# Kernel optimization log

Measured on AMD Instinct MI355X. Metric: run time of the kernel, lower is better.

## Reference

```python
import jax, jax.numpy as jnp
import numpy as np

D_MODEL = 96
D_INNER = 192   # ssm_ratio * d_model
R = 6           # dt_rank = ceil(96/16)
DH = 32         # d_inner // dt_rank (per-head dim)
K = 4           # scan directions
N = 16          # d_state
EPS = 1e-5


def setup_inputs() -> dict:
    key = jax.random.key(0)
    ks = jax.random.split(key, 10)
    B, H, W = 8, 64, 64
    f = lambda k, s, sc: jax.random.normal(k, s, jnp.float32) * sc
    return dict(
        x=jax.random.normal(ks[0], (B, H, W, D_MODEL), jnp.float32),
        w_in=f(ks[1], (D_MODEL, D_INNER), 0.02),
        w_conv=f(ks[2], (3, 3, 1, D_INNER), 0.1),      # depthwise HWIO
        b_conv=f(ks[3], (D_INNER,), 0.1),
        x_proj_weight=f(ks[4], (K, R + 2 * N, D_INNER), 0.02),
        A_logs=f(ks[5], (K, R), 0.5),
        Ds=jnp.ones((K, R, DH), jnp.float32),
        dt_bias=0.1 * jax.random.uniform(ks[6], (K, R), jnp.float32),
        ln_g=jnp.ones((D_INNER,), jnp.float32),
        ln_b=jnp.zeros((D_INNER,), jnp.float32),
        w_out=f(ks[7], (D_INNER, D_MODEL), 0.02),
    )


def _cross_scan(x):
    # x: (B,H,W,C) -> (B,L,4,C): [row-major, col-major, rev row, rev col]
    B, H, W, C = x.shape
    x0 = x.reshape(B, H * W, C)
    x1 = jnp.transpose(x, (0, 2, 1, 3)).reshape(B, H * W, C)
    return jnp.stack([x0, x1, x0[:, ::-1], x1[:, ::-1]], axis=2)


def _cross_merge(ys, H, W):
    # ys: (B,L,4,C) -> (B,L,C) summed after undoing each scan order
    B, L, _, C = ys.shape
    y_row = ys[:, :, 0] + ys[:, :, 2][:, ::-1]
    y_col = ys[:, :, 1] + ys[:, :, 3][:, ::-1]
    y_col = jnp.transpose(y_col.reshape(B, W, H, C), (0, 2, 1, 3)).reshape(B, L, C)
    return y_row + y_col


def _selective_scan(us, dts, As, Bs, Cs, Dsr, dtb):
    # us:(B,L,KR,DH) dts:(B,L,KR) As:(KR,) Bs,Cs:(B,L,K,N) Dsr:(KR,DH) dtb:(KR,)
    dt = jax.nn.softplus(dts + dtb)                 # (B,L,KR)
    decay = jnp.exp(dt * As)                        # (B,L,KR)
    xu = dt[..., None] * us                         # (B,L,KR,DH)
    Bh = jnp.repeat(Bs, R, axis=2)                  # (B,L,KR,N) head h -> group h//R
    Ch = jnp.repeat(Cs, R, axis=2)
    B_, L, KR, _ = us.shape
    tfirst = lambda a: jnp.moveaxis(a, 1, 0)

    def step(h, inp):
        dec, xu_t, b_t, c_t = inp                   # (B,KR),(B,KR,DH),(B,KR,N),(B,KR,N)
        h = dec[:, :, None, None] * h + xu_t[..., None] * b_t[:, :, None, :]
        y = jnp.einsum('bkdn,bkn->bkd', h, c_t)
        return h, y

    h0 = jnp.zeros((B_, KR, DH, N), us.dtype)
    _, ys = jax.lax.scan(step, h0, (tfirst(decay), tfirst(xu), tfirst(Bh), tfirst(Ch)))
    ys = jnp.moveaxis(ys, 0, 1)                     # (B,L,KR,DH)
    return ys + us * Dsr                            # skip term D*u


def reference(x, w_in, w_conv, b_conv, x_proj_weight, A_logs, Ds, dt_bias, ln_g, ln_b, w_out):
    B, H, W, _ = x.shape
    L = H * W
    xi = x @ w_in                                   # in_proj (no bias)
    xi = jax.lax.conv_general_dilated(
        xi, w_conv, (1, 1), 'SAME', feature_group_count=D_INNER,
        dimension_numbers=('NHWC', 'HWIO', 'NHWC')) + b_conv
    xi = jax.nn.silu(xi)
    xs = _cross_scan(xi)                            # (B,L,4,D_INNER)
    x_dbl = jnp.einsum('blkd,kcd->blkc', xs, x_proj_weight)
    dts = x_dbl[..., :R].reshape(B, L, K * R)
    Bs = x_dbl[..., R:R + N]                        # (B,L,K,N)
    Cs = x_dbl[..., R + N:]
    us = xs.reshape(B, L, K * R, DH)
    As = -jnp.exp(A_logs.astype(jnp.float32)).reshape(K * R)
    Dsr = Ds.reshape(K * R, DH)
    dtb = dt_bias.reshape(K * R)
    ys = _selective_scan(us, dts, As, Bs, Cs, Dsr, dtb)   # (B,L,KR,DH)
    y = _cross_merge(ys.reshape(B, L, K, R * DH), H, W)   # (B,L,D_INNER)
    mu = y.mean(-1, keepdims=True)
    var = ((y - mu) ** 2).mean(-1, keepdims=True)
    y = (y - mu) / jnp.sqrt(var + EPS) * ln_g + ln_b
    y = y.reshape(B, H, W, D_INNER)
    return y @ w_out                                # out_proj (no bias)
```

## Files before the change

### kernel.cpp

```cpp
#include <hip/hip_runtime.h>
#include <hip/hip_bf16.h>

#define BB 8
#define LL 4096
#define DM 96
#define DI 192
#define RRR 6
#define DHH 32
#define KKK 4
#define NNN 16
#define KRR 24
#define NCH 64
#define TT 64
#define RST 48

__device__ __forceinline__ float softplus_f(float x){
    float ax = fabsf(x);
    return fmaxf(x, 0.f) + __logf(1.f + __expf(-ax));
}
__device__ __forceinline__ float silu_f(float x){ return x / (1.f + __expf(-x)); }

__global__ void k0p(const float* __restrict__ W, const float* __restrict__ g,
                    const float* __restrict__ bta, const float* __restrict__ w_out,
                    float* __restrict__ WpR, float* __restrict__ wg, float* __restrict__ sgbw){
    int i = blockIdx.x * 256 + threadIdx.x;
    if (i < DI * 160){
        int d = i / 160, cc = i % 160; int gq = cc / 40, nc = cc % 40;
        int dir = (gq == 0) ? 0 : (gq == 1) ? 2 : (gq == 2) ? 1 : 3;
        float v = 0.f;
        if (nc < 6) v = W[(dir * 38 + nc) * DI + d];
        else if (nc >= 8) v = W[(dir * 38 + (nc - 2)) * DI + d];
        WpR[i] = v;
    } else if (i < DI * 160 + DI * DM){
        int j = i - DI * 160; int c = j / DM;
        wg[j] = w_out[j] * g[c];
    } else if (i < DI * 160 + DI * DM + DM){
        int m = i - (DI * 160 + DI * DM);
        float s = 0.f, t = 0.f;
        for (int c = 0; c < DI; ++c){
            float w = w_out[c * DM + m];
            s = fmaf(g[c], w, s);
            t = fmaf(bta[c], w, t);
        }
        sgbw[m] = s; sgbw[DM + m] = t;
    }
}

__global__ __launch_bounds__(384) void k1_inproj(const float* __restrict__ x,
                                                 const float* __restrict__ w_in,
                                                 float* __restrict__ xw){
    __shared__ float xT[DM][68];
    int pix0 = blockIdx.x * 64;
    for (int i = threadIdx.x; i < 64 * DM; i += 384){
        int c = i % DM, p = i / DM;
        xT[c][p] = x[(size_t)(pix0 + p) * DM + c];
    }
    __syncthreads();
    int cg = threadIdx.x % 48, pg = threadIdx.x / 48;
    int p0 = pg * 8;
    float4 acc[8];
    #pragma unroll
    for (int i = 0; i < 8; ++i) acc[i] = make_float4(0.f, 0.f, 0.f, 0.f);
    const float* wcol = w_in + cg * 4;
    for (int d = 0; d < DM; ++d){
        float4 w4 = *(const float4*)(wcol + d * DI);
        float4 xa = *(const float4*)(&xT[d][p0]);
        float4 xb = *(const float4*)(&xT[d][p0 + 4]);
        float xs[8] = {xa.x, xa.y, xa.z, xa.w, xb.x, xb.y, xb.z, xb.w};
        #pragma unroll
        for (int pi = 0; pi < 8; ++pi){
            acc[pi].x = fmaf(xs[pi], w4.x, acc[pi].x);
            acc[pi].y = fmaf(xs[pi], w4.y, acc[pi].y);
            acc[pi].z = fmaf(xs[pi], w4.z, acc[pi].z);
            acc[pi].w = fmaf(xs[pi], w4.w, acc[pi].w);
        }
    }
    #pragma unroll
    for (int pi = 0; pi < 8; ++pi)
        *(float4*)(xw + (size_t)(pix0 + p0 + pi) * DI + cg * 4) = acc[pi];
}

__global__ void k2_conv(const float* __restrict__ xw, const float* __restrict__ wc,
                        const float* __restrict__ bc, float* __restrict__ xi,
                        float* __restrict__ xiT){
    int gid = blockIdx.x * 256 + threadIdx.x;
    int c4 = gid % 48; int pix = gid / 48;
    int b = pix >> 12; int l = pix & 4095; int h = l >> 6; int w = l & 63;
    int c = c4 * 4;
    float4 acc = *(const float4*)(bc + c);
    #pragma unroll
    for (int dh = 0; dh < 3; ++dh){
        int hh = h + dh - 1; if ((unsigned)hh >= 64u) continue;
        #pragma unroll
        for (int dw = 0; dw < 3; ++dw){
            int ww2 = w + dw - 1; if ((unsigned)ww2 >= 64u) continue;
            float4 tap = *(const float4*)(xw + (size_t)((b << 12) + (hh << 6) + ww2) * DI + c);
            float4 wv  = *(const float4*)(wc + (dh * 3 + dw) * DI + c);
            acc.x = fmaf(tap.x, wv.x, acc.x);
            acc.y = fmaf(tap.y, wv.y, acc.y);
            acc.z = fmaf(tap.z, wv.z, acc.z);
            acc.w = fmaf(tap.w, wv.w, acc.w);
        }
    }
    acc.x = silu_f(acc.x); acc.y = silu_f(acc.y); acc.z = silu_f(acc.z); acc.w = silu_f(acc.w);
    *(float4*)(xi + (size_t)pix * DI + c) = acc;
    int lT = ((l & 63) << 6) | (l >> 6);
    *(float4*)(xiT + (size_t)((b << 12) + lT) * DI + c) = acc;
}

__global__ __launch_bounds__(320) void k3seq(const float* __restrict__ xi,
                                             const float* __restrict__ xiT,
                                             const float* __restrict__ WpR,
                                             const float* __restrict__ A_logs,
                                             const float* __restrict__ dtb,
                                             float* __restrict__ rec){
    __shared__ float xT[DI][65];
    int pass = blockIdx.y, b = blockIdx.z;
    const float* src = (pass ? xiT : xi) + (((size_t)b) << 12) * DI;
    int p0blk = blockIdx.x * 64;
    for (int i = threadIdx.x; i < 64 * DI; i += 320){
        int c = i % DI, p = i / DI;
        xT[c][p] = src[(size_t)(p0blk + p) * DI + c];
    }
    __syncthreads();
    int kg = threadIdx.x % 20, pg = threadIdx.x / 20;
    int p0 = pg * 4;
    float4 acc[4];
    #pragma unroll
    for (int i = 0; i < 4; ++i) acc[i] = make_float4(0.f, 0.f, 0.f, 0.f);
    const float* wcol = WpR + pass * 80 + kg * 4;
    for (int d = 0; d < DI; ++d){
        float4 w4 = *(const float4*)(wcol + d * 160);
        float4 xv = *(const float4*)(&xT[d][p0]);
        float xs[4] = {xv.x, xv.y, xv.z, xv.w};
        #pragma unroll
        for (int pi = 0; pi < 4; ++pi){
            acc[pi].x = fmaf(xs[pi], w4.x, acc[pi].x);
            acc[pi].y = fmaf(xs[pi], w4.y, acc[pi].y);
            acc[pi].z = fmaf(xs[pi], w4.z, acc[pi].z);
            acc[pi].w = fmaf(xs[pi], w4.w, acc[pi].w);
        }
    }
    int gq = kg / 10;
    int dir = (pass == 0) ? (gq == 0 ? 0 : 2) : (gq == 0 ? 1 : 3);
    int nc0 = (kg % 10) * 4;
    float* rb = rec + (size_t)(b * KKK + dir) * LL * RST;
    float A0, A1, A2, A3, b0, b1, b2, b3;
    if (nc0 == 0){
        A0 = -__expf(A_logs[dir * RRR + 0]); b0 = dtb[dir * RRR + 0];
        A1 = -__expf(A_logs[dir * RRR + 1]); b1 = dtb[dir * RRR + 1];
        A2 = -__expf(A_logs[dir * RRR + 2]); b2 = dtb[dir * RRR + 2];
        A3 = -__expf(A_logs[dir * RRR + 3]); b3 = dtb[dir * RRR + 3];
    } else if (nc0 == 4){
        A0 = -__expf(A_logs[dir * RRR + 4]); b0 = dtb[dir * RRR + 4];
        A1 = -__expf(A_logs[dir * RRR + 5]); b1 = dtb[dir * RRR + 5];
    }
    #pragma unroll
    for (int pi = 0; pi < 4; ++pi){
        int gp = p0blk + p0 + pi;
        int t = (dir < 2) ? gp : (LL - 1 - gp);
        float* rw = rb + (size_t)t * RST;
        float4 v = acc[pi];
        if (nc0 == 0){
            float4 dt4, dc4;
            dt4.x = softplus_f(v.x + b0); dc4.x = __expf(dt4.x * A0);
            dt4.y = softplus_f(v.y + b1); dc4.y = __expf(dt4.y * A1);
            dt4.z = softplus_f(v.z + b2); dc4.z = __expf(dt4.z * A2);
            dt4.w = softplus_f(v.w + b3); dc4.w = __expf(dt4.w * A3);
            *(float4*)(rw + 0) = dt4;
            *(float4*)(rw + 8) = dc4;
        } else if (nc0 == 4){
            float4 dt4, dc4;
            dt4.x = softplus_f(v.x + b0); dc4.x = __expf(dt4.x * A0);
            dt4.y = softplus_f(v.y + b1); dc4.y = __expf(dt4.y * A1);
            dt4.z = 0.f; dt4.w = 0.f; dc4.z = 0.f; dc4.w = 0.f;
            *(float4*)(rw + 4)  = dt4;
            *(float4*)(rw + 12) = dc4;
        } else {
            *(float4*)(rw + nc0 + 8) = v;
        }
    }
}

__global__ __launch_bounds__(192) void k4a(const float* __restrict__ xi, const float* __restrict__ xiT,
                                           const float* __restrict__ rec,
                                           float* __restrict__ Pb, float* __restrict__ Sb){
    int chunk = blockIdx.x, k = blockIdx.y, b = blockIdx.z;
    int r = threadIdx.x >> 5, d = threadIdx.x & 31;
    int kr = k * RRR + r;
    const float* rp = rec + ((size_t)(b * KKK + k) * LL + chunk * TT) * RST;
    const float* xb = ((k & 1) ? xiT : xi) + (((size_t)b) << 12) * DI + r * DHH + d;
    const float* up; ptrdiff_t ust;
    if (k < 2){ up = xb + (size_t)(chunk * TT) * DI;          ust = DI;  }
    else      { up = xb + (size_t)(LL - 1 - chunk * TT) * DI; ust = -(ptrdiff_t)DI; }
    float h[NNN];
    #pragma unroll
    for (int n = 0; n < NNN; ++n) h[n] = 0.f;
    float P = 1.f;
    #pragma unroll 4
    for (int tt = 0; tt < TT; ++tt){
        float dt  = rp[r];
        float dec = rp[8 + r];
        float u = *up;
        float xu = dt * u;
        P *= dec;
        float Bv[NNN];
        *(float4*)(Bv + 0)  = *(const float4*)(rp + 16);
        *(float4*)(Bv + 4)  = *(const float4*)(rp + 20);
        *(float4*)(Bv + 8)  = *(const float4*)(rp + 24);
        *(float4*)(Bv + 12) = *(const float4*)(rp + 28);
        #pragma unroll
        for (int n = 0; n < NNN; ++n) h[n] = fmaf(dec, h[n], xu * Bv[n]);
        rp += RST; up += ust;
    }
    size_t sb = (((size_t)(b * KRR + kr) * NCH + chunk) * DHH + d) * NNN;
    #pragma unroll
    for (int n = 0; n < NNN; ++n) Sb[sb + n] = h[n];
    if (d == 0) Pb[(size_t)(b * KRR + kr) * NCH + chunk] = P;
}

__global__ __launch_bounds__(512) void k4b(const float* __restrict__ Pb, float* __restrict__ Sb){
    int scan = blockIdx.x;
    int tid = threadIdx.x;
    size_t base = (size_t)scan * NCH * 512 + tid;
    const float* Pp = Pb + (size_t)scan * NCH;
    float s[NCH];
    #pragma unroll
    for (int c = 0; c < NCH; ++c) s[c] = Sb[base + (size_t)c * 512];
    float hb = 0.f;
    #pragma unroll
    for (int c = 0; c < NCH; ++c){
        float nv = fmaf(Pp[c], hb, s[c]);
        Sb[base + (size_t)c * 512] = hb;
        hb = nv;
    }
}

__global__ __launch_bounds__(192) void k4c(const float* __restrict__ xi, const float* __restrict__ xiT,
                                           const float* __restrict__ rec,
                                           const float* __restrict__ Ds, const float* __restrict__ Sb,
                                           __hip_bfloat16* __restrict__ ybuf){
    int chunk = blockIdx.x, k = blockIdx.y, b = blockIdx.z;
    int r = threadIdx.x >> 5, d = threadIdx.x & 31;
    int kr = k * RRR + r;
    float Dv = Ds[kr * DHH + d];
    float h[NNN];
    size_t sb = (((size_t)(b * KRR + kr) * NCH + chunk) * DHH + d) * NNN;
    #pragma unroll
    for (int n = 0; n < NNN; ++n) h[n] = Sb[sb + n];
    const float* rp = rec + ((size_t)(b * KKK + k) * LL + chunk * TT) * RST;
    const float* xb = ((k & 1) ? xiT : xi) + (((size_t)b) << 12) * DI + r * DHH + d;
    const float* up; ptrdiff_t ust;
    if (k < 2){ up = xb + (size_t)(chunk * TT) * DI;          ust = DI;  }
    else      { up = xb + (size_t)(LL - 1 - chunk * TT) * DI; ust = -(ptrdiff_t)DI; }
    __hip_bfloat16* yp = ybuf + ((size_t)(k * BB + b) * LL + chunk * TT) * DI + r * DHH + d;
    #pragma unroll 2
    for (int tt = 0; tt < TT; ++tt){
        float dt  = rp[r];
        float dec = rp[8 + r];
        float u = *up;
        float xu = dt * u;
        float Bv[NNN], Cv[NNN];
        *(float4*)(Bv + 0)  = *(const float4*)(rp + 16);
        *(float4*)(Bv + 4)  = *(const float4*)(rp + 20);
        *(float4*)(Bv + 8)  = *(const float4*)(rp + 24);
        *(float4*)(Bv + 12) = *(const float4*)(rp + 28);
        *(float4*)(Cv + 0)  = *(const float4*)(rp + 32);
        *(float4*)(Cv + 4)  = *(const float4*)(rp + 36);
        *(float4*)(Cv + 8)  = *(const float4*)(rp + 40);
        *(float4*)(Cv + 12) = *(const float4*)(rp + 44);
        float y = 0.f;
        #pragma unroll
        for (int n = 0; n < NNN; ++n){
            h[n] = fmaf(dec, h[n], xu * Bv[n]);
            y = fmaf(h[n], Cv[n], y);
        }
        y = fmaf(u, Dv, y);
        *yp = __float2bfloat16(y);
        rp += RST; up += ust; yp += DI;
    }
}

__global__ __launch_bounds__(256) void k5_out(const __hip_bfloat16* __restrict__ ybuf,
                       const float* __restrict__ wg, const float* __restrict__ sgbw,
                       float* __restrict__ out){
    __shared__ float yT[DI][36];
    __shared__ float rsL[32], rmL[32];
    int pix0 = blockIdx.x * 32;
    int b = pix0 >> 12;
    int l0 = pix0 & 4095;
    const __hip_bfloat16* y0 = ybuf + (size_t)(0 * BB + b) * LL * DI;
    const __hip_bfloat16* y1 = ybuf + (size_t)(1 * BB + b) * LL * DI;
    const __hip_bfloat16* y2 = ybuf + (size_t)(2 * BB + b) * LL * DI;
    const __hip_bfloat16* y3 = ybuf + (size_t)(3 * BB + b) * LL * DI;
    for (int i = threadIdx.x; i < 32 * DI; i += 256){
        int c = i % DI, p = i / DI;
        int l = l0 + p; int hh = l >> 6, ww = l & 63;
        int lT = (ww << 6) | hh;
        float s = __bfloat162float(y0[(size_t)l * DI + c])
                + __bfloat162float(y2[(size_t)(LL - 1 - l) * DI + c])
                + __bfloat162float(y1[(size_t)lT * DI + c])
                + __bfloat162float(y3[(size_t)(LL - 1 - lT) * DI + c]);
        yT[c][p] = s;
    }
    __syncthreads();
    {
        int p = threadIdx.x >> 3, cg = threadIdx.x & 7;
        float s = 0.f, s2 = 0.f;
        for (int c = cg; c < DI; c += 8){ float v = yT[c][p]; s += v; s2 = fmaf(v, v, s2); }
        s += __shfl_xor(s, 1, 64); s2 += __shfl_xor(s2, 1, 64);
        s += __shfl_xor(s, 2, 64); s2 += __shfl_xor(s2, 2, 64);
        s += __shfl_xor(s, 4, 64); s2 += __shfl_xor(s2, 4, 64);
        if (cg == 0){
            float mu = s * (1.f / DI);
            float var = s2 * (1.f / DI) - mu * mu;
            float rs = rsqrtf(var + 1e-5f);
            rsL[p] = rs; rmL[p] = rs * mu;
        }
    }
    __syncthreads();
    if (threadIdx.x < 192){
        int mg = threadIdx.x % 24, pg = threadIdx.x / 24;
        int p0 = pg * 4;
        float4 acc[4];
        #pragma unroll
        for (int i = 0; i < 4; ++i) acc[i] = make_float4(0.f, 0.f, 0.f, 0.f);
        const float* wcol = wg + mg * 4;
        for (int c = 0; c < DI; ++c){
            float4 w4 = *(const float4*)(wcol + c * DM);
            float4 yv = *(const float4*)(&yT[c][p0]);
            float ys[4] = {yv.x, yv.y, yv.z, yv.w};
            #pragma unroll
            for (int pi = 0; pi < 4; ++pi){
                acc[pi].x = fmaf(ys[pi], w4.x, acc[pi].x);
                acc[pi].y = fmaf(ys[pi], w4.y, acc[pi].y);
                acc[pi].z = fmaf(ys[pi], w4.z, acc[pi].z);
                acc[pi].w = fmaf(ys[pi], w4.w, acc[pi].w);
            }
        }
        float4 sg4 = *(const float4*)(sgbw + mg * 4);
        float4 bw4 = *(const float4*)(sgbw + DM + mg * 4);
        #pragma unroll
        for (int pi = 0; pi < 4; ++pi){
            float rs = rsL[p0 + pi], rm = rmL[p0 + pi];
            float4 o;
            o.x = fmaf(acc[pi].x, rs, fmaf(-rm, sg4.x, bw4.x));
            o.y = fmaf(acc[pi].y, rs, fmaf(-rm, sg4.y, bw4.y));
            o.z = fmaf(acc[pi].z, rs, fmaf(-rm, sg4.z, bw4.z));
            o.w = fmaf(acc[pi].w, rs, fmaf(-rm, sg4.w, bw4.w));
            *(float4*)(out + (size_t)(pix0 + p0 + pi) * DM + mg * 4) = o;
        }
    }
}

extern "C" void kernel_launch(void* const* d_in, const int* in_sizes, int n_in,
                              void* d_out, int out_size, void* d_ws, size_t ws_size,
                              hipStream_t stream){
    const float* x      = (const float*)d_in[0];
    const float* w_in   = (const float*)d_in[1];
    const float* w_conv = (const float*)d_in[2];
    const float* b_conv = (const float*)d_in[3];
    const float* xproj  = (const float*)d_in[4];
    const float* A_logs = (const float*)d_in[5];
    const float* Ds     = (const float*)d_in[6];
    const float* dtbias = (const float*)d_in[7];
    const float* ln_g   = (const float*)d_in[8];
    const float* ln_b   = (const float*)d_in[9];
    const float* w_out  = (const float*)d_in[10];
    float* out = (float*)d_out;

    float* ws   = (float*)d_ws;
    float* xi   = ws;
    float* xiT  = xi + 6291456;
    float* Sb   = xiT + 6291456;
    float* Pb   = Sb + 6291456;
    float* WpR  = Pb + 16384;
    float* wg   = WpR + 30720;
    float* sgbw = wg + 18432;
    float* big  = sgbw + 192;
    float* xw   = big;
    float* rec  = big;
    __hip_bfloat16* ybuf = (__hip_bfloat16*)(big + 6291456);

    k0p<<<193, 256, 0, stream>>>(xproj, ln_g, ln_b, w_out, WpR, wg, sgbw);
    k1_inproj<<<512, 384, 0, stream>>>(x, w_in, xw);
    k2_conv<<<6144, 256, 0, stream>>>(xw, w_conv, b_conv, xi, xiT);
    k3seq<<<dim3(64, 2, BB), 320, 0, stream>>>(xi, xiT, WpR, A_logs, dtbias, rec);
    k4a<<<dim3(NCH, KKK, BB), 192, 0, stream>>>(xi, xiT, rec, Pb, Sb);
    k4b<<<192, 512, 0, stream>>>(Pb, Sb);
    k4c<<<dim3(NCH, KKK, BB), 192, 0, stream>>>(xi, xiT, rec, Ds, Sb, ybuf);
    k5_out<<<1024, 256, 0, stream>>>(ybuf, wg, sgbw, out);
}
```

Measured before the change: 308.4 us.

## Merge x_proj passes, vectorize smem staging loads, split chunk-scan blocks

The x_proj kernel now reads only the row-major xi once per pixel tile and computes all four directions' projections in one block. For the transposed directions it remaps each output row through the index transpose, so the duplicate read of xiT is gone. Both projection kernels stage input into shared memory with float4 loads, and k3seq stages it in two halves to keep shared memory small. The inter-chunk scan kernel is split into twice as many 256-thread blocks to spread work across more CUs. The costs are scattered writes for the transposed directions and larger per-thread accumulators, which raise register pressure.

```diff
diff --git a/kernel.cpp b/kernel.cpp
--- a/kernel.cpp
+++ b/kernel.cpp
@@ -51,9 +51,11 @@
                                                  float* __restrict__ xw){
     __shared__ float xT[DM][68];
     int pix0 = blockIdx.x * 64;
-    for (int i = threadIdx.x; i < 64 * DM; i += 384){
-        int c = i % DM, p = i / DM;
-        xT[c][p] = x[(size_t)(pix0 + p) * DM + c];
+    for (int i = threadIdx.x; i < 64 * 24; i += 384){
+        int c4 = i % 24, p = i / 24;
+        float4 v = *(const float4*)(x + (size_t)(pix0 + p) * DM + c4 * 4);
+        xT[c4 * 4 + 0][p] = v.x; xT[c4 * 4 + 1][p] = v.y;
+        xT[c4 * 4 + 2][p] = v.z; xT[c4 * 4 + 3][p] = v.w;
     }
     __syncthreads();
     int cg = threadIdx.x % 48, pg = threadIdx.x / 48;
@@ -109,43 +111,50 @@
 }
 
 __global__ __launch_bounds__(320) void k3seq(const float* __restrict__ xi,
-                                             const float* __restrict__ xiT,
                                              const float* __restrict__ WpR,
                                              const float* __restrict__ A_logs,
                                              const float* __restrict__ dtb,
                                              float* __restrict__ rec){
-    __shared__ float xT[DI][65];
-    int pass = blockIdx.y, b = blockIdx.z;
-    const float* src = (pass ? xiT : xi) + (((size_t)b) << 12) * DI;
-    int p0blk = blockIdx.x * 64;
-    for (int i = threadIdx.x; i < 64 * DI; i += 320){
-        int c = i % DI, p = i / DI;
-        xT[c][p] = src[(size_t)(p0blk + p) * DI + c];
-    }
-    __syncthreads();
-    int kg = threadIdx.x % 20, pg = threadIdx.x / 20;
-    int p0 = pg * 4;
-    float4 acc[4];
-    #pragma unroll
-    for (int i = 0; i < 4; ++i) acc[i] = make_float4(0.f, 0.f, 0.f, 0.f);
-    const float* wcol = WpR + pass * 80 + kg * 4;
-    for (int d = 0; d < DI; ++d){
-        float4 w4 = *(const float4*)(wcol + d * 160);
-        float4 xv = *(const float4*)(&xT[d][p0]);
-        float xs[4] = {xv.x, xv.y, xv.z, xv.w};
-        #pragma unroll
-        for (int pi = 0; pi < 4; ++pi){
-            acc[pi].x = fmaf(xs[pi], w4.x, acc[pi].x);
-            acc[pi].y = fmaf(xs[pi], w4.y, acc[pi].y);
-            acc[pi].z = fmaf(xs[pi], w4.z, acc[pi].z);
-            acc[pi].w = fmaf(xs[pi], w4.w, acc[pi].w);
+    __shared__ float xT[96][68];
+    int b = blockIdx.y;
+    int l0 = blockIdx.x * 64;
+    const float* src = xi + ((((size_t)b) << 12) + l0) * DI;
+    int kg = threadIdx.x % 40, pg = threadIdx.x / 40;
+    int p0 = pg * 8;
+    float4 acc[8];
+    #pragma unroll
+    for (int i = 0; i < 8; ++i) acc[i] = make_float4(0.f, 0.f, 0.f, 0.f);
+    const float* wcol = WpR + kg * 4;
+    #pragma unroll
+    for (int half = 0; half < 2; ++half){
+        __syncthreads();
+        for (int i = threadIdx.x; i < 64 * 24; i += 320){
+            int c4 = i % 24, p = i / 24;
+            float4 v = *(const float4*)(src + (size_t)p * DI + half * 96 + c4 * 4);
+            xT[c4 * 4 + 0][p] = v.x; xT[c4 * 4 + 1][p] = v.y;
+            xT[c4 * 4 + 2][p] = v.z; xT[c4 * 4 + 3][p] = v.w;
+        }
+        __syncthreads();
+        const float* w = wcol + half * 96 * 160;
+        for (int d = 0; d < 96; ++d){
+            float4 w4 = *(const float4*)(w + d * 160);
+            float4 xa = *(const float4*)(&xT[d][p0]);
+            float4 xb = *(const float4*)(&xT[d][p0 + 4]);
+            float xs[8] = {xa.x, xa.y, xa.z, xa.w, xb.x, xb.y, xb.z, xb.w};
+            #pragma unroll
+            for (int pi = 0; pi < 8; ++pi){
+                acc[pi].x = fmaf(xs[pi], w4.x, acc[pi].x);
+                acc[pi].y = fmaf(xs[pi], w4.y, acc[pi].y);
+                acc[pi].z = fmaf(xs[pi], w4.z, acc[pi].z);
+                acc[pi].w = fmaf(xs[pi], w4.w, acc[pi].w);
+            }
         }
     }
     int gq = kg / 10;
-    int dir = (pass == 0) ? (gq == 0 ? 0 : 2) : (gq == 0 ? 1 : 3);
+    int dir = (gq == 0) ? 0 : (gq == 1) ? 2 : (gq == 2) ? 1 : 3;
     int nc0 = (kg % 10) * 4;
     float* rb = rec + (size_t)(b * KKK + dir) * LL * RST;
-    float A0, A1, A2, A3, b0, b1, b2, b3;
+    float A0 = 0.f, A1 = 0.f, A2 = 0.f, A3 = 0.f, b0 = 0.f, b1 = 0.f, b2 = 0.f, b3 = 0.f;
     if (nc0 == 0){
         A0 = -__expf(A_logs[dir * RRR + 0]); b0 = dtb[dir * RRR + 0];
         A1 = -__expf(A_logs[dir * RRR + 1]); b1 = dtb[dir * RRR + 1];
@@ -156,9 +165,14 @@
         A1 = -__expf(A_logs[dir * RRR + 5]); b1 = dtb[dir * RRR + 5];
     }
     #pragma unroll
-    for (int pi = 0; pi < 4; ++pi){
-        int gp = p0blk + p0 + pi;
-        int t = (dir < 2) ? gp : (LL - 1 - gp);
+    for (int pi = 0; pi < 8; ++pi){
+        int l = l0 + p0 + pi;
+        int lT = ((l & 63) << 6) | (l >> 6);
+        int t;
+        if (dir == 0) t = l;
+        else if (dir == 2) t = LL - 1 - l;
+        else if (dir == 1) t = lT;
+        else t = LL - 1 - lT;
         float* rw = rb + (size_t)t * RST;
         float4 v = acc[pi];
         if (nc0 == 0){
@@ -219,9 +233,10 @@
     if (d == 0) Pb[(size_t)(b * KRR + kr) * NCH + chunk] = P;
 }
 
-__global__ __launch_bounds__(512) void k4b(const float* __restrict__ Pb, float* __restrict__ Sb){
-    int scan = blockIdx.x;
-    int tid = threadIdx.x;
+__global__ __launch_bounds__(256) void k4b(const float* __restrict__ Pb, float* __restrict__ Sb){
+    int scan = blockIdx.x >> 1;
+    int half = blockIdx.x & 1;
+    int tid = half * 256 + threadIdx.x;
     size_t base = (size_t)scan * NCH * 512 + tid;
     const float* Pp = Pb + (size_t)scan * NCH;
     float s[NCH];
@@ -385,9 +400,9 @@
     k0p<<<193, 256, 0, stream>>>(xproj, ln_g, ln_b, w_out, WpR, wg, sgbw);
     k1_inproj<<<512, 384, 0, stream>>>(x, w_in, xw);
     k2_conv<<<6144, 256, 0, stream>>>(xw, w_conv, b_conv, xi, xiT);
-    k3seq<<<dim3(64, 2, BB), 320, 0, stream>>>(xi, xiT, WpR, A_logs, dtbias, rec);
+    k3seq<<<dim3(64, BB), 320, 0, stream>>>(xi, WpR, A_logs, dtbias, rec);
     k4a<<<dim3(NCH, KKK, BB), 192, 0, stream>>>(xi, xiT, rec, Pb, Sb);
-    k4b<<<192, 512, 0, stream>>>(Pb, Sb);
+    k4b<<<384, 256, 0, stream>>>(Pb, Sb);
     k4c<<<dim3(NCH, KKK, BB), 192, 0, stream>>>(xi, xiT, rec, Ds, Sb, ybuf);
     k5_out<<<1024, 256, 0, stream>>>(ybuf, wg, sgbw, out);
 }
```

Measured after the change: 277.1 us. 1.11x faster.
